# Kernel optimization log

Hardware: AMD Instinct MI355X
Metric: run time of the kernel (lower is better)

The kernel has to match this reference:

```python
import jax, jax.numpy as jnp
import numpy as np

# Dimensions
B, H, W, C = 2, 256, 256, 32   # batch, height, width, in-channels
P = 8                          # patch_size
HEADS = 8                      # no_heads
DIM = 32                       # per-head channel dim (== C so residual works w/o Conv1x1)
GH, GW = H // P, W // P        # patch grid


def _ln(x, scale, bias, eps=1e-6):
    # flax LayerNorm over last axis, eps=1e-6
    mu = jnp.mean(x, axis=-1, keepdims=True)
    var = jnp.var(x, axis=-1, keepdims=True)
    return (x - mu) * jax.lax.rsqrt(var + eps) * scale + bias


def _patch_conv(x, Wk, b):
    # Conv kernel=PxP stride=PxP; H,W divisible by P so SAME == VALID
    y = jax.lax.conv_general_dilated(x, Wk, (P, P), 'VALID',
                                     dimension_numbers=('NHWC', 'HWIO', 'NHWC'))
    return y + b


def _proj_heads(x, Wk, b):
    # LinearProjection with no_heads: [B,H,W,C] -> [B,HEADS,H,W,DIM]
    y = _patch_conv(x, Wk, b)                       # [B,GH,GW,DIM*P*P*HEADS]
    y = y.reshape(B, GH, GW, DIM, P, P, HEADS)      # (c p0 p1 head) unpack
    y = y.transpose(0, 6, 1, 4, 2, 5, 3)            # b head gh p0 gw p1 c
    return y.reshape(B, HEADS, H, W, DIM)


def _x_to_patch(x):
    # [B,HEADS,H,W,DIM] -> [B,HEADS,DIM,GH,GW,P,P]
    y = x.reshape(B, HEADS, GH, P, GW, P, DIM)
    return y.transpose(0, 1, 6, 2, 4, 3, 5)


def _patch_to_x(x):
    # [B,HEADS,DIM,GH,GW,P,P] -> [B,HEADS,H,W,DIM]
    y = x.transpose(0, 1, 3, 5, 4, 6, 2)            # b head gh p1 gw p2 c
    return y.reshape(B, HEADS, H, W, DIM)


def setup_inputs() -> dict:
    key = jax.random.key(0)
    ks = jax.random.split(key, 8)
    F = DIM * P * P * HEADS  # qkv conv output features = 16384
    s_qkv = 0.02
    return {
        'x': jax.random.normal(ks[0], (B, H, W, C), jnp.float32),
        'ln1_scale': jnp.ones((C,), jnp.float32),
        'ln1_bias': jnp.zeros((C,), jnp.float32),
        'Wq': jax.random.normal(ks[1], (P, P, C, F), jnp.float32) * s_qkv,
        'bq': jnp.zeros((F,), jnp.float32),
        'Wk': jax.random.normal(ks[2], (P, P, C, F), jnp.float32) * s_qkv,
        'bk': jnp.zeros((F,), jnp.float32),
        'Wv': jax.random.normal(ks[3], (P, P, C, F), jnp.float32) * s_qkv,
        'bv': jnp.zeros((F,), jnp.float32),
        'ln2_scale': jnp.ones((DIM,), jnp.float32),
        'ln2_bias': jnp.zeros((DIM,), jnp.float32),
        'Wo': jax.random.normal(ks[4], (P, P, HEADS * DIM, DIM * P * P), jnp.float32) * s_qkv,
        'bo': jnp.zeros((DIM * P * P,), jnp.float32),
    }


def reference(x, ln1_scale, ln1_bias, Wq, bq, Wk, bk, Wv, bv,
              ln2_scale, ln2_bias, Wo, bo):
    # FrequencyTransformer (encoder=True, mlp=False): LN -> FSAS -> +residual
    xn = _ln(x, ln1_scale, ln1_bias)

    q = _proj_heads(xn, Wq, bq)                     # [B,HEADS,H,W,DIM]
    k = _proj_heads(xn, Wk, bk)
    v = _proj_heads(xn, Wv, bv)

    q_fft = jnp.fft.rfft2(_x_to_patch(q))           # [B,HEADS,DIM,GH,GW,P,P//2+1]
    k_fft = jnp.fft.rfft2(_x_to_patch(k))
    out = jnp.fft.irfft2(q_fft * k_fft, s=(P, P))   # frequency dot product
    out = _patch_to_x(out)                          # [B,HEADS,H,W,DIM]
    out = _ln(out, ln2_scale, ln2_bias)

    o = v * out                                     # elementwise gate by V
    # b head h w c -> b h w (head c)
    o = o.transpose(0, 2, 3, 1, 4).reshape(B, H, W, HEADS * DIM)

    # output LinearProjection (no_heads=None)
    y = _patch_conv(o, Wo, bo)                      # [B,GH,GW,DIM*P*P]
    y = y.reshape(B, GH, GW, DIM, P, P)
    y = y.transpose(0, 1, 4, 2, 5, 3).reshape(B, H, W, DIM)

    return y + x                                    # residual (DIM == C)
```

## Files before the change

### kernel.cpp

```cpp
#include <hip/hip_runtime.h>
#include <hip/hip_bf16.h>
#include <cstdint>

typedef __bf16 bf16_t;
typedef __attribute__((ext_vector_type(8))) __bf16 bf16x8;
typedef __attribute__((ext_vector_type(4))) float f32x4;

__device__ __forceinline__ float b2f(ushort u) {
    union { float f; uint32_t i; } x; x.i = ((uint32_t)u) << 16; return x.f;
}
__device__ __forceinline__ ushort f2b(float f) {
    uint32_t i = __builtin_bit_cast(uint32_t, f);
    uint32_t r = (i + 0x7FFFu + ((i >> 16) & 1u)) >> 16;
    return (ushort)r;
}

__device__ __forceinline__ void g2l16(const ushort* gp, ushort* lp) {
    __builtin_amdgcn_global_load_lds(
        (const __attribute__((address_space(1))) uint32_t*)gp,
        (__attribute__((address_space(3))) uint32_t*)lp, 16, 0, 0);
}

__global__ __launch_bounds__(256) void ln1_pack(
    const float* __restrict__ x, const float* __restrict__ g,
    const float* __restrict__ b, ushort* __restrict__ A1) {
    int pix = blockIdx.x * 256 + threadIdx.x;
    const float4* xp = (const float4*)(x + (size_t)pix * 32);
    float v[32]; float s = 0.f;
#pragma unroll
    for (int i = 0; i < 8; ++i) {
        float4 f = xp[i];
        v[i*4+0] = f.x; v[i*4+1] = f.y; v[i*4+2] = f.z; v[i*4+3] = f.w;
        s += f.x + f.y + f.z + f.w;
    }
    float mu = s * (1.f/32.f), s2 = 0.f;
#pragma unroll
    for (int i = 0; i < 32; ++i) { float d = v[i]-mu; s2 += d*d; }
    float inv = rsqrtf(s2 * (1.f/32.f) + 1e-6f);
    int w = pix & 255, h = (pix >> 8) & 255, bb = pix >> 16;
    size_t row = ((size_t)bb*32 + (h>>3))*32 + (w>>3);
    ushort* dst = A1 + row*2048 + (size_t)((h&7)*8 + (w&7))*32;
    ushort o[32];
#pragma unroll
    for (int i = 0; i < 32; ++i) o[i] = f2b((v[i]-mu)*inv*g[i] + b[i]);
    uint4* d4 = (uint4*)dst; const uint4* s4 = (const uint4*)o;
#pragma unroll
    for (int i = 0; i < 4; ++i) d4[i] = s4[i];
}

__global__ __launch_bounds__(256) void wcvt(
    const float* __restrict__ W, ushort* __restrict__ WT, int K, int N) {
    __shared__ float tile[64][65];
    int n0 = blockIdx.x * 64, k0 = blockIdx.y * 64;
    int t = threadIdx.x;
    int col4 = (t & 15) * 4, krow = t >> 4;
#pragma unroll
    for (int it = 0; it < 4; ++it) {
        int kk = it*16 + krow;
        float4 f = *(const float4*)(W + (size_t)(k0+kk)*N + n0 + col4);
        tile[kk][col4+0] = f.x; tile[kk][col4+1] = f.y;
        tile[kk][col4+2] = f.z; tile[kk][col4+3] = f.w;
    }
    __syncthreads();
    int n = t >> 2, ch = t & 3;
    ushort o[16];
#pragma unroll
    for (int i = 0; i < 16; ++i) o[i] = f2b(tile[ch*16 + i][n]);
    uint4* dst = (uint4*)(WT + (size_t)(n0+n)*K + k0 + ch*16);
    dst[0] = ((const uint4*)o)[0];
    dst[1] = ((const uint4*)o)[1];
}

template <int EPI>
__global__ __launch_bounds__(512, 2) void gemm256(
    const ushort* __restrict__ A, const ushort* __restrict__ Bt,
    const float* __restrict__ bias, ushort* __restrict__ Cb,
    float* __restrict__ Out, int M, int N, int K, int KS) {
    __shared__ __align__(16) ushort sA[32768];
    __shared__ __align__(16) ushort sB[32768];
    const int tid  = threadIdx.x;
    const int wave = tid >> 6, lane = tid & 63;
    const int lrow = lane & 15, lquad = lane >> 4;
    const int wm = wave >> 2, wn = wave & 3;

    const int nwg  = gridDim.x;
    const int flat = blockIdx.x;
    const int swz  = (flat & 7) * (nwg >> 3) + (flat >> 3);
    const int m0 = (swz & 7) * 256;
    const int n0 = (swz >> 3) * 256;

    const int kb  = (EPI == 1) ? blockIdx.z * KS : 0;
    const int NTl = KS >> 5;

    const int seg0 = wave * 2, seg1 = seg0 + 1;
    const ushort* aS0 = A  + (size_t)(m0 + (seg0 >> 2)*64 + lane)*K + kb + (seg0 & 3)*8;
    const ushort* aS1 = A  + (size_t)(m0 + (seg1 >> 2)*64 + lane)*K + kb + (seg1 & 3)*8;
    const ushort* bS0 = Bt + (size_t)(n0 + (seg0 >> 2)*64 + lane)*K + kb + (seg0 & 3)*8;
    const ushort* bS1 = Bt + (size_t)(n0 + (seg1 >> 2)*64 + lane)*K + kb + (seg1 & 3)*8;
    ushort* aD0 = sA + (seg0 & 3)*2048 + (seg0 >> 2)*512;
    ushort* aD1 = sA + (seg1 & 3)*2048 + (seg1 >> 2)*512;
    ushort* bD0 = sB + (seg0 & 3)*2048 + (seg0 >> 2)*512;
    ushort* bD1 = sB + (seg1 & 3)*2048 + (seg1 >> 2)*512;

    const ushort* pA = sA + lquad*2048 + (wm*128 + lrow)*8;
    const ushort* pB = sB + lquad*2048 + (wn*64  + lrow)*8;

    f32x4 acc[8][4];
#pragma unroll
    for (int i = 0; i < 8; ++i)
#pragma unroll
        for (int j = 0; j < 4; ++j) acc[i][j] = f32x4{0.f, 0.f, 0.f, 0.f};

#define STAGE(TI) { const int _b = (TI) & 3; const size_t _ko = (size_t)(TI) * 32; \
    g2l16(aS0 + _ko, aD0 + _b*8192); g2l16(aS1 + _ko, aD1 + _b*8192);              \
    g2l16(bS0 + _ko, bD0 + _b*8192); g2l16(bS1 + _ko, bD1 + _b*8192); }

    STAGE(0); STAGE(1); STAGE(2);
    asm volatile("s_waitcnt vmcnt(8)\n\ts_barrier" ::: "memory");

    for (int ti = 0; ti < NTl; ++ti) {
        if (ti + 3 < NTl) STAGE(ti + 3);
        const ushort* bufA = pA + (ti & 3) * 8192;
        const ushort* bufB = pB + (ti & 3) * 8192;
        bf16x8 af[8], bg[4];
#pragma unroll
        for (int i = 0; i < 8; ++i)
            af[i] = __builtin_bit_cast(bf16x8, *(const uint4*)(bufA + i*128));
#pragma unroll
        for (int j = 0; j < 4; ++j)
            bg[j] = __builtin_bit_cast(bf16x8, *(const uint4*)(bufB + j*128));
        __builtin_amdgcn_s_setprio(1);
#pragma unroll
        for (int i = 0; i < 8; ++i)
#pragma unroll
            for (int j = 0; j < 4; ++j)
                acc[i][j] = __builtin_amdgcn_mfma_f32_16x16x32_bf16(
                    af[i], bg[j], acc[i][j], 0, 0, 0);
        __builtin_amdgcn_s_setprio(0);
        if (ti + 3 < NTl)      asm volatile("s_waitcnt vmcnt(8)\n\ts_barrier" ::: "memory");
        else if (ti + 2 < NTl) asm volatile("s_waitcnt vmcnt(4)\n\ts_barrier" ::: "memory");
        else if (ti + 1 < NTl) asm volatile("s_waitcnt vmcnt(0)\n\ts_barrier" ::: "memory");
    }
#undef STAGE

    if constexpr (EPI == 0) {
        float bvj[4];
#pragma unroll
        for (int j = 0; j < 4; ++j) bvj[j] = bias[n0 + wn*64 + j*16 + lrow];
        __syncthreads();
        ushort* warena = sA + wave * 2048;
#pragma unroll
        for (int pass = 0; pass < 4; ++pass) {
#pragma unroll
            for (int ih = 0; ih < 2; ++ih) {
                const int i = pass*2 + ih;
#pragma unroll
                for (int j = 0; j < 4; ++j)
#pragma unroll
                    for (int re = 0; re < 4; ++re) {
                        int mrow = ih*16 + lquad*4 + re;
                        int col  = j*16 + lrow;
                        warena[mrow*64 + col] = f2b(acc[i][j][re] + bvj[j]);
                    }
            }
#pragma unroll
            for (int t2 = 0; t2 < 4; ++t2) {
                int chunk = t2*64 + lane;
                int row = chunk >> 3, seg = chunk & 7;
                uint4 v = *(const uint4*)&warena[row*64 + seg*8];
                *(uint4*)&Cb[(size_t)(m0 + wm*128 + pass*32 + row)*N
                             + n0 + wn*64 + seg*8] = v;
            }
        }
    } else {
        float* P = Out + (size_t)blockIdx.z * M * N;
#pragma unroll
        for (int j = 0; j < 4; ++j) {
            int n = n0 + wn*64 + j*16 + lrow;
#pragma unroll
            for (int i = 0; i < 8; ++i) {
                int mbase = m0 + wm*128 + i*16 + lquad*4;
#pragma unroll
                for (int re = 0; re < 4; ++re)
                    P[(size_t)(mbase + re)*N + n] = acc[i][j][re];
            }
        }
    }
}

__global__ __launch_bounds__(256, 3) void conv_gate(
    const ushort* __restrict__ Qb, const ushort* __restrict__ Kb,
    const ushort* __restrict__ Vb, const float* __restrict__ ln2_s,
    const float* __restrict__ ln2_b, ushort* __restrict__ A2) {
    __shared__ ushort sT[64 * 258];
    const int t = threadIdx.x;
    const int m = blockIdx.x;
    const int c = t & 31, h = t >> 5;
    const ushort* Qrow = Qb + (size_t)m * 16384;
    const ushort* Krow = Kb + (size_t)m * 16384;
    const ushort* Vrow = Vb + (size_t)m * 16384;

#define STAGE_T(SRC)                                                        \
    {                                                                       \
        _Pragma("unroll")                                                   \
        for (int it = 0; it < 8; ++it) {                                    \
            int ci = it*256 + t;                                            \
            int p = ci & 63, cc = ci >> 6;                                  \
            uint4 w = ((const uint4*)(SRC))[ci];                            \
            uint uu[4] = {w.x, w.y, w.z, w.w};                              \
            _Pragma("unroll")                                               \
            for (int e = 0; e < 4; ++e) {                                   \
                sT[p*258 + (2*e  )*32 + cc] = (ushort)(uu[e] & 0xffffu);    \
                sT[p*258 + (2*e+1)*32 + cc] = (ushort)(uu[e] >> 16);        \
            }                                                               \
        }                                                                   \
    }

    float q[64];
    STAGE_T(Qrow);
    __syncthreads();
#pragma unroll
    for (int p = 0; p < 64; ++p) q[p] = b2f(sT[p*258 + t]);
    __syncthreads();
    STAGE_T(Krow);
    __syncthreads();
#undef STAGE_T

    const float scl = ln2_s[c], bia = ln2_b[c];
    ushort* A2row = A2 + (size_t)m * 16384;
    const ushort* vbase = Vrow + c*512 + h;

#pragma unroll
    for (int p0 = 0; p0 < 8; ++p0) {
        ushort vraw[8];
#pragma unroll
        for (int p1 = 0; p1 < 8; ++p1) vraw[p1] = vbase[p0*64 + p1*8];

        float o[8];
#pragma unroll
        for (int p1 = 0; p1 < 8; ++p1) o[p1] = 0.f;
#pragma unroll
        for (int b0 = 0; b0 < 8; ++b0) {
            const int qr = ((p0 - b0) & 7) * 8;
#pragma unroll
            for (int b1 = 0; b1 < 8; ++b1) {
                float kv = b2f(sT[(b0*8 + b1)*258 + t]);
#pragma unroll
                for (int p1 = 0; p1 < 8; ++p1)
                    o[p1] += kv * q[qr + ((p1 - b1) & 7)];
            }
        }

        float s1[8], s2[8];
#pragma unroll
        for (int p1 = 0; p1 < 8; ++p1) { s1[p1] = o[p1]; s2[p1] = o[p1]*o[p1]; }
#pragma unroll
        for (int mask = 1; mask <= 16; mask <<= 1) {
#pragma unroll
            for (int p1 = 0; p1 < 8; ++p1) {
                s1[p1] += __shfl_xor(s1[p1], mask, 64);
                s2[p1] += __shfl_xor(s2[p1], mask, 64);
            }
        }
#pragma unroll
        for (int p1 = 0; p1 < 8; ++p1) {
            float mu  = s1[p1] * 0.03125f;
            float var = s2[p1] * 0.03125f - mu * mu;
            float inv = rsqrtf(var + 1e-6f);
            float on  = (o[p1] - mu) * inv * scl + bia;
            A2row[(p0*8 + p1)*256 + t] = f2b(b2f(vraw[p1]) * on);
        }
    }
}

__global__ __launch_bounds__(256) void reduce_out(
    const float* __restrict__ Pp, const float* __restrict__ x,
    const float* __restrict__ bo, float* __restrict__ out) {
    __shared__ float sn[32*65];
    const int t = threadIdx.x, m = blockIdx.x;
    float4 s0 = {0.f,0.f,0.f,0.f}, s1 = {0.f,0.f,0.f,0.f};
#pragma unroll
    for (int z = 0; z < 4; ++z) {
        const float4* base =
            (const float4*)(Pp + ((size_t)z*2048 + m) * 2048);
        float4 u = base[t], v = base[256 + t];
        s0.x += u.x; s0.y += u.y; s0.z += u.z; s0.w += u.w;
        s1.x += v.x; s1.y += v.y; s1.z += v.z; s1.w += v.w;
    }
    {
        int na = t*4;
        int nb = (256 + t)*4;
        float va[4] = {s0.x, s0.y, s0.z, s0.w};
        float vb[4] = {s1.x, s1.y, s1.z, s1.w};
#pragma unroll
        for (int e = 0; e < 4; ++e) {
            int n1 = na + e, n2 = nb + e;
            sn[(n1 >> 6)*65 + (n1 & 63)] = va[e];
            sn[(n2 >> 6)*65 + (n2 & 63)] = vb[e];
        }
    }
    __syncthreads();
    const int c = t & 31, pi = t >> 5;
    const int bb = m >> 10, gh = (m >> 5) & 31, gw = m & 31;
#pragma unroll
    for (int it = 0; it < 8; ++it) {
        int p = it*8 + pi;
        int p0 = p >> 3, p1 = p & 7;
        int n = c*64 + p;
        size_t oi = ((size_t)((bb*256 + gh*8 + p0)*256 + gw*8 + p1))*32 + c;
        out[oi] = x[oi] + bo[n] + sn[c*65 + p];
    }
}

extern "C" void kernel_launch(void* const* d_in, const int* in_sizes, int n_in,
                              void* d_out, int out_size, void* d_ws, size_t ws_size,
                              hipStream_t stream) {
    (void)in_sizes; (void)n_in; (void)out_size; (void)ws_size;
    const float* x    = (const float*)d_in[0];
    const float* ln1s = (const float*)d_in[1];
    const float* ln1b = (const float*)d_in[2];
    const float* Wq   = (const float*)d_in[3];
    const float* bq   = (const float*)d_in[4];
    const float* Wk   = (const float*)d_in[5];
    const float* bk   = (const float*)d_in[6];
    const float* Wv   = (const float*)d_in[7];
    const float* bv   = (const float*)d_in[8];
    const float* ln2s = (const float*)d_in[9];
    const float* ln2b = (const float*)d_in[10];
    const float* Wo   = (const float*)d_in[11];
    const float* bo   = (const float*)d_in[12];
    float* out = (float*)d_out;

    char* ws = (char*)d_ws;
    ushort* A1 = (ushort*)(ws);
    ushort* WT = (ushort*)(ws + 8388608);
    ushort* Qb = (ushort*)(ws + 75497472);
    ushort* Kb = (ushort*)(ws + 142606336);
    ushort* Vb = (ushort*)(ws + 209715200);
    ushort* A2 = Qb;
    float*  Pp = (float*)Kb;

    ln1_pack<<<512, 256, 0, stream>>>(x, ln1s, ln1b, A1);

    wcvt<<<dim3(256, 32), 256, 0, stream>>>(Wq, WT, 2048, 16384);
    gemm256<0><<<dim3(512, 1, 1), 512, 0, stream>>>(A1, WT, bq, Qb, nullptr,
                                                    2048, 16384, 2048, 2048);
    wcvt<<<dim3(256, 32), 256, 0, stream>>>(Wk, WT, 2048, 16384);
    gemm256<0><<<dim3(512, 1, 1), 512, 0, stream>>>(A1, WT, bk, Kb, nullptr,
                                                    2048, 16384, 2048, 2048);
    wcvt<<<dim3(256, 32), 256, 0, stream>>>(Wv, WT, 2048, 16384);
    gemm256<0><<<dim3(512, 1, 1), 512, 0, stream>>>(A1, WT, bv, Vb, nullptr,
                                                    2048, 16384, 2048, 2048);

    conv_gate<<<2048, 256, 0, stream>>>(Qb, Kb, Vb, ln2s, ln2b, A2);

    wcvt<<<dim3(32, 256), 256, 0, stream>>>(Wo, WT, 16384, 2048);
    gemm256<1><<<dim3(64, 1, 4), 512, 0, stream>>>(A2, WT, nullptr, nullptr, Pp,
                                                   2048, 2048, 16384, 4096);
    reduce_out<<<2048, 256, 0, stream>>>(Pp, x, bo, out);
}
```

Baseline: 1.659 ms.

## Split GEMM main loop into two MFMA phases interleaved with staged A/B loads

Splits each k-tile iteration of the bf16 GEMM into two halves. The A-tile global-to-LDS prefetch is issued between the first fragment reads and MFMAs, and the B-tile prefetch between the second, with extra barriers and lgkmcnt waits around each phase. The aim is to spread memory issue across compute and hide LDS read latency. It also replaces the XOR-style workgroup swizzle with a different block-to-tile mapping that groups 8 N-tiles by 8 M-tiles for L2 reuse. The added barriers and waits per iteration may add synchronisation stalls.

```diff
diff --git a/kernel.cpp b/kernel.cpp
--- a/kernel.cpp
+++ b/kernel.cpp
@@ -83,11 +83,9 @@
     const int lrow = lane & 15, lquad = lane >> 4;
     const int wm = wave >> 2, wn = wave & 3;
 
-    const int nwg  = gridDim.x;
-    const int flat = blockIdx.x;
-    const int swz  = (flat & 7) * (nwg >> 3) + (flat >> 3);
-    const int m0 = (swz & 7) * 256;
-    const int n0 = (swz >> 3) * 256;
+    const int blk = blockIdx.x;
+    const int m0 = ((blk >> 3) & 7) * 256;
+    const int n0 = (((blk >> 6) << 3) + (blk & 7)) * 256;
 
     const int kb  = (EPI == 1) ? blockIdx.z * KS : 0;
     const int NTl = KS >> 5;
@@ -111,37 +109,59 @@
 #pragma unroll
         for (int j = 0; j < 4; ++j) acc[i][j] = f32x4{0.f, 0.f, 0.f, 0.f};
 
-#define STAGE(TI) { const int _b = (TI) & 3; const size_t _ko = (size_t)(TI) * 32; \
-    g2l16(aS0 + _ko, aD0 + _b*8192); g2l16(aS1 + _ko, aD1 + _b*8192);              \
+#define STAGE_A(TI) { const int _b = (TI) & 3; const size_t _ko = (size_t)(TI) * 32; \
+    g2l16(aS0 + _ko, aD0 + _b*8192); g2l16(aS1 + _ko, aD1 + _b*8192); }
+#define STAGE_B(TI) { const int _b = (TI) & 3; const size_t _ko = (size_t)(TI) * 32; \
     g2l16(bS0 + _ko, bD0 + _b*8192); g2l16(bS1 + _ko, bD1 + _b*8192); }
 
-    STAGE(0); STAGE(1); STAGE(2);
+    STAGE_A(0); STAGE_B(0); STAGE_A(1); STAGE_B(1); STAGE_A(2); STAGE_B(2);
     asm volatile("s_waitcnt vmcnt(8)\n\ts_barrier" ::: "memory");
 
     for (int ti = 0; ti < NTl; ++ti) {
-        if (ti + 3 < NTl) STAGE(ti + 3);
         const ushort* bufA = pA + (ti & 3) * 8192;
         const ushort* bufB = pB + (ti & 3) * 8192;
-        bf16x8 af[8], bg[4];
-#pragma unroll
-        for (int i = 0; i < 8; ++i)
-            af[i] = __builtin_bit_cast(bf16x8, *(const uint4*)(bufA + i*128));
+        const bool st = (ti + 3 < NTl);
+        bf16x8 af0[4], af1[4], bg[4];
+#pragma unroll
+        for (int i = 0; i < 4; ++i)
+            af0[i] = __builtin_bit_cast(bf16x8, *(const uint4*)(bufA + i*128));
 #pragma unroll
         for (int j = 0; j < 4; ++j)
             bg[j] = __builtin_bit_cast(bf16x8, *(const uint4*)(bufB + j*128));
+        if (st) STAGE_A(ti + 3);
+        asm volatile("s_barrier" ::: "memory");
+        asm volatile("s_waitcnt lgkmcnt(0)" ::: "memory");
+        __builtin_amdgcn_sched_barrier(0);
         __builtin_amdgcn_s_setprio(1);
 #pragma unroll
-        for (int i = 0; i < 8; ++i)
+        for (int i = 0; i < 4; ++i)
 #pragma unroll
             for (int j = 0; j < 4; ++j)
                 acc[i][j] = __builtin_amdgcn_mfma_f32_16x16x32_bf16(
-                    af[i], bg[j], acc[i][j], 0, 0, 0);
+                    af0[i], bg[j], acc[i][j], 0, 0, 0);
+        __builtin_amdgcn_s_setprio(0);
+        asm volatile("s_barrier" ::: "memory");
+#pragma unroll
+        for (int i = 0; i < 4; ++i)
+            af1[i] = __builtin_bit_cast(bf16x8, *(const uint4*)(bufA + (4+i)*128));
+        if (st) STAGE_B(ti + 3);
+        asm volatile("s_barrier" ::: "memory");
+        asm volatile("s_waitcnt lgkmcnt(0)" ::: "memory");
+        __builtin_amdgcn_sched_barrier(0);
+        __builtin_amdgcn_s_setprio(1);
+#pragma unroll
+        for (int i = 0; i < 4; ++i)
+#pragma unroll
+            for (int j = 0; j < 4; ++j)
+                acc[4+i][j] = __builtin_amdgcn_mfma_f32_16x16x32_bf16(
+                    af1[i], bg[j], acc[4+i][j], 0, 0, 0);
         __builtin_amdgcn_s_setprio(0);
         if (ti + 3 < NTl)      asm volatile("s_waitcnt vmcnt(8)\n\ts_barrier" ::: "memory");
         else if (ti + 2 < NTl) asm volatile("s_waitcnt vmcnt(4)\n\ts_barrier" ::: "memory");
         else if (ti + 1 < NTl) asm volatile("s_waitcnt vmcnt(0)\n\ts_barrier" ::: "memory");
     }
-#undef STAGE
+#undef STAGE_A
+#undef STAGE_B
 
     if constexpr (EPI == 0) {
         float bvj[4];
```

Result: faster. 1.349 ms (-18.7%).
